# Performance work log

Hardware: AMD Instinct MI355X
Metric: run time of the kernel (lower is better)

The kernel has to match this reference:

```python
import jax, jax.numpy as jnp
import numpy as np

Q, N = 8, 256          # number of sub-networks, state dim per network
QN = Q * N             # 2048 total state dimension
BS = 128               # batch size
TMAX = 128             # time steps
STEP = 0.01            # Euler integration step size


def _offdiag_block_mask(q, n):
    # L_mask: ones everywhere except the q diagonal n x n blocks
    diag_blocks = np.kron(np.eye(q), np.ones((n, n)))
    return jnp.asarray(1.0 - diag_blocks, dtype=jnp.float32)


def setup_inputs() -> dict:
    key = jax.random.key(0)
    ks = jax.random.split(key, 6)
    s = 1.0 / np.sqrt(QN)  # keep 128-step Euler recurrence numerically tame
    X0 = jax.random.normal(ks[0], (BS, QN), dtype=jnp.float32)
    A = jax.random.normal(ks[1], (QN, QN), dtype=jnp.float32) * s
    B = jax.random.normal(ks[2], (QN, QN), dtype=jnp.float32) * s
    W = jax.random.normal(ks[3], (QN, QN), dtype=jnp.float32) * s
    # P is block-diagonal and well-conditioned (I + small block-diag noise)
    blk = np.kron(np.eye(Q), np.ones((N, N))).astype(np.float32)
    P = jnp.eye(QN, dtype=jnp.float32) + 0.1 * jax.random.normal(ks[4], (QN, QN), dtype=jnp.float32) * jnp.asarray(blk)
    bx = jax.random.normal(ks[5], (QN,), dtype=jnp.float32)
    return {"X0": X0, "A": A, "B": B, "W": W, "P": P, "bx": bx, "tmax": TMAX}


def reference(X0, A, B, W, P, bx, tmax):
    # mask GL weight to off-block-diagonal coupling, then L = W - P^{-1} W^T P
    Wm = W * _offdiag_block_mask(Q, N)
    L = Wm - jnp.linalg.solve(P, Wm.T @ P)
    M = A + L                      # (qn, qn)
    Xi0 = X0.T                     # (qn, bs)
    b = bx[:, None]                # (qn, 1) broadcast over batch

    def step_fn(Xi, _):
        Xn = Xi + STEP * (M @ Xi + B @ jax.nn.relu(Xi) + b)
        return Xn, Xn

    _, Xs = jax.lax.scan(step_fn, Xi0, None, length=tmax - 1)  # (tmax-1, qn, bs)
    X = jnp.concatenate([Xi0[None], Xs], axis=0)               # (tmax, qn, bs)
    return jnp.transpose(X, (2, 0, 1))                          # (bs, tmax, qn)
```

## Files before the change

kernel.cpp:

```cpp
#include <hip/hip_runtime.h>

typedef unsigned short u16;
typedef __attribute__((ext_vector_type(8))) short bf16x8;
typedef __attribute__((ext_vector_type(4))) float f32x4;
typedef __attribute__((ext_vector_type(4))) unsigned short u16x4;

#define QN    2048
#define BSZ   128
#define TMAXK 128
#define STEPF 0.01f
#define NEWTON_ITERS 46

#define GLOAD_LDS16(gsrc, ldst) \
  __builtin_amdgcn_global_load_lds((const __attribute__((address_space(1))) void*)(gsrc), \
                                   (__attribute__((address_space(3))) void*)(ldst), 16, 0, 0)

__device__ __forceinline__ u16 f2bf(float f){
  unsigned u = __float_as_uint(f);
  u += 0x7fffu + ((u >> 16) & 1u);
  return (u16)(u >> 16);
}
__device__ __forceinline__ float bf2f(u16 h){
  return __uint_as_float(((unsigned)h) << 16);
}


__global__ __launch_bounds__(256) void alpha_k(const float* __restrict__ P, float* __restrict__ alpha){
  int q = blockIdx.x, i = threadIdx.x;
  const float* Pb = P + (size_t)(q << 8) * QN + (q << 8);
  float rs = 0.f, cs = 0.f;
  for (int c = 0; c < 256; ++c){
    rs += fabsf(Pb[(size_t)i * QN + c]);
    cs += fabsf(Pb[(size_t)c * QN + i]);
  }
  __shared__ float red[256];
  red[i] = rs; __syncthreads();
  for (int o = 128; o > 0; o >>= 1){ if (i < o) red[i] = fmaxf(red[i], red[i+o]); __syncthreads(); }
  float mr = red[0];
  __syncthreads();
  red[i] = cs; __syncthreads();
  for (int o = 128; o > 0; o >>= 1){ if (i < o) red[i] = fmaxf(red[i], red[i+o]); __syncthreads(); }
  if (i == 0) alpha[q] = mr * red[0];
}

__global__ __launch_bounds__(256) void initV_k(const float* __restrict__ P, const float* __restrict__ alpha, float* __restrict__ V){
  int idx = blockIdx.x * 256 + threadIdx.x;
  int q = idx >> 16, rc = idx & 65535;
  int r = rc >> 8, c = rc & 255;
  V[idx] = P[(size_t)((q << 8) + c) * QN + (q << 8) + r] / alpha[q];
}

__global__ __launch_bounds__(256) void newton_TV_k(const float* __restrict__ P,
                                                   const float* __restrict__ Vin,
                                                   float* __restrict__ Vout){
  int q = blockIdx.x >> 4, st = blockIdx.x & 15;
  int cb = st << 4;
  const float* Pb = P + (size_t)(q << 8) * QN + (q << 8);
  const float* Vb = Vin + (q << 16);
  __shared__ float Asm[16][256];
  __shared__ float Bsm[16][16];
  __shared__ float Tb[256][16];
  int tid = threadIdx.x, ty = tid >> 2, tx = tid & 3;
  float acc[4][4];

#pragma unroll
  for (int i = 0; i < 4; i++)
#pragma unroll
    for (int j = 0; j < 4; j++) acc[i][j] = 0.f;
  for (int kb = 0; kb < 256; kb += 16){
    f32x4 av[4];
#pragma unroll
    for (int rd = 0; rd < 4; ++rd){
      int idx = rd * 256 + tid;
      int row = idx >> 2, kq = (idx & 3) << 2;
      av[rd] = *(const f32x4*)(Pb + (size_t)row * QN + kb + kq);
    }
    float bv = Vb[(size_t)(kb + (tid >> 4)) * 256 + cb + (tid & 15)];
    __syncthreads();
#pragma unroll
    for (int rd = 0; rd < 4; ++rd){
      int idx = rd * 256 + tid;
      int row = idx >> 2, kq = (idx & 3) << 2;
#pragma unroll
      for (int u = 0; u < 4; ++u) Asm[kq + u][row] = av[rd][u];
    }
    Bsm[tid >> 4][tid & 15] = bv;
    __syncthreads();
#pragma unroll
    for (int kk = 0; kk < 16; kk++){
      f32x4 a = *(const f32x4*)&Asm[kk][ty << 2];
      f32x4 b = *(const f32x4*)&Bsm[kk][tx << 2];
#pragma unroll
      for (int i = 0; i < 4; i++)
#pragma unroll
        for (int j = 0; j < 4; j++) acc[i][j] += a[i] * b[j];
    }
  }
#pragma unroll
  for (int i = 0; i < 4; i++){
    f32x4 o; o.x = acc[i][0]; o.y = acc[i][1]; o.z = acc[i][2]; o.w = acc[i][3];
    *(f32x4*)&Tb[(ty << 2) + i][tx << 2] = o;
  }

#pragma unroll
  for (int i = 0; i < 4; i++)
#pragma unroll
    for (int j = 0; j < 4; j++) acc[i][j] = 0.f;
  for (int kb = 0; kb < 256; kb += 16){
    f32x4 av[4];
#pragma unroll
    for (int rd = 0; rd < 4; ++rd){
      int idx = rd * 256 + tid;
      int row = idx >> 2, kq = (idx & 3) << 2;
      av[rd] = *(const f32x4*)(Vb + (size_t)row * 256 + kb + kq);
    }
    __syncthreads();
#pragma unroll
    for (int rd = 0; rd < 4; ++rd){
      int idx = rd * 256 + tid;
      int row = idx >> 2, kq = (idx & 3) << 2;
#pragma unroll
      for (int u = 0; u < 4; ++u) Asm[kq + u][row] = av[rd][u];
    }
    __syncthreads();
#pragma unroll
    for (int kk = 0; kk < 16; kk++){
      f32x4 a = *(const f32x4*)&Asm[kk][ty << 2];
      f32x4 b = *(const f32x4*)&Tb[kb + kk][tx << 2];
#pragma unroll
      for (int i = 0; i < 4; i++)
#pragma unroll
        for (int j = 0; j < 4; j++) acc[i][j] += a[i] * b[j];
    }
  }
  float* Ob = Vout + (q << 16);
#pragma unroll
  for (int i = 0; i < 4; i++){
    int row = (ty << 2) + i;
    f32x4 vo = *(const f32x4*)(Vb + (size_t)row * 256 + cb + (tx << 2));
    f32x4 o;
    o.x = 2.f*vo.x - acc[i][0]; o.y = 2.f*vo.y - acc[i][1];
    o.z = 2.f*vo.z - acc[i][2]; o.w = 2.f*vo.w - acc[i][3];
    *(f32x4*)(Ob + (size_t)row * 256 + cb + (tx << 2)) = o;
  }
}

__global__ __launch_bounds__(256) void build_Y_k(const float* __restrict__ W, const float* __restrict__ P, float* __restrict__ Ymat){
  int j  = blockIdx.x >> 7;
  int rt = (blockIdx.x >> 2) & 31;
  int ct = blockIdx.x & 3;
  int rb = rt << 6, cb = ct << 6, jb = j << 8;
  int tid = threadIdx.x, ty = tid >> 4, tx = tid & 15;
  if ((rt >> 2) == j){
#pragma unroll
    for (int i = 0; i < 4; i++){
      f32x4 z = {0.f, 0.f, 0.f, 0.f};
      *(f32x4*)(Ymat + (size_t)(rb + (ty << 2) + i) * QN + jb + cb + (tx << 2)) = z;
    }
    return;
  }
  __shared__ float Asm[16][68];
  __shared__ float Bsm[16][68];
  float acc[4][4];
#pragma unroll
  for (int i = 0; i < 4; i++)
#pragma unroll
    for (int j2 = 0; j2 < 4; j2++) acc[i][j2] = 0.f;
  int sr = tid & 63, sk = tid >> 6;
  for (int kb = 0; kb < 256; kb += 16){
    float a0 = W[(size_t)(jb + kb + sk     ) * QN + rb + sr];
    float a1 = W[(size_t)(jb + kb + sk +  4) * QN + rb + sr];
    float a2 = W[(size_t)(jb + kb + sk +  8) * QN + rb + sr];
    float a3 = W[(size_t)(jb + kb + sk + 12) * QN + rb + sr];
    float b0 = P[(size_t)(jb + kb + sk     ) * QN + jb + cb + sr];
    float b1 = P[(size_t)(jb + kb + sk +  4) * QN + jb + cb + sr];
    float b2 = P[(size_t)(jb + kb + sk +  8) * QN + jb + cb + sr];
    float b3 = P[(size_t)(jb + kb + sk + 12) * QN + jb + cb + sr];
    __syncthreads();
    Asm[sk   ][sr] = a0; Asm[sk+ 4][sr] = a1; Asm[sk+ 8][sr] = a2; Asm[sk+12][sr] = a3;
    Bsm[sk   ][sr] = b0; Bsm[sk+ 4][sr] = b1; Bsm[sk+ 8][sr] = b2; Bsm[sk+12][sr] = b3;
    __syncthreads();
#pragma unroll
    for (int kk = 0; kk < 16; kk++){
      f32x4 a = *(const f32x4*)&Asm[kk][ty << 2];
      f32x4 b = *(const f32x4*)&Bsm[kk][tx << 2];
#pragma unroll
      for (int i = 0; i < 4; i++)
#pragma unroll
        for (int j2 = 0; j2 < 4; j2++) acc[i][j2] += a[i] * b[j2];
    }
  }
#pragma unroll
  for (int i = 0; i < 4; i++){
    f32x4 o; o.x = acc[i][0]; o.y = acc[i][1]; o.z = acc[i][2]; o.w = acc[i][3];
    *(f32x4*)(Ymat + (size_t)(rb + (ty << 2) + i) * QN + jb + cb + (tx << 2)) = o;
  }
}

__global__ __launch_bounds__(256) void build_C_k(const float* __restrict__ Vfin, const float* __restrict__ Ymat,
                                                 const float* __restrict__ Ain, const float* __restrict__ W,
                                                 u16* __restrict__ C1, u16* __restrict__ C2){
  int ib = blockIdx.x >> 7;
  int rest = blockIdx.x & 127;
  int rt = rest >> 5, ct = rest & 31;
  int rb = rt << 6, cb = ct << 6;
  const float* Ab = Vfin + (ib << 16);
  __shared__ float Asm[16][68];
  __shared__ float Bsm[16][68];
  int tid = threadIdx.x, ty = tid >> 4, tx = tid & 15;
  float acc[4][4];
#pragma unroll
  for (int i = 0; i < 4; i++)
#pragma unroll
    for (int j = 0; j < 4; j++) acc[i][j] = 0.f;
  int ar = tid >> 2, ak = (tid & 3) << 2;
  int bc = tid & 63, bk = tid >> 6;
  for (int kb = 0; kb < 256; kb += 16){
    f32x4 av = *(const f32x4*)(Ab + (size_t)(rb + ar) * 256 + kb + ak);
    float b0 = Ymat[(size_t)((ib << 8) + kb + bk     ) * QN + cb + bc];
    float b1 = Ymat[(size_t)((ib << 8) + kb + bk +  4) * QN + cb + bc];
    float b2 = Ymat[(size_t)((ib << 8) + kb + bk +  8) * QN + cb + bc];
    float b3 = Ymat[(size_t)((ib << 8) + kb + bk + 12) * QN + cb + bc];
    __syncthreads();
    Asm[ak+0][ar] = av.x; Asm[ak+1][ar] = av.y; Asm[ak+2][ar] = av.z; Asm[ak+3][ar] = av.w;
    Bsm[bk   ][bc] = b0;  Bsm[bk+ 4][bc] = b1;  Bsm[bk+ 8][bc] = b2;  Bsm[bk+12][bc] = b3;
    __syncthreads();
#pragma unroll
    for (int kk = 0; kk < 16; kk++){
      f32x4 a = *(const f32x4*)&Asm[kk][ty << 2];
      f32x4 b = *(const f32x4*)&Bsm[kk][tx << 2];
#pragma unroll
      for (int i = 0; i < 4; i++)
#pragma unroll
        for (int j = 0; j < 4; j++) acc[i][j] += a[i] * b[j];
    }
  }
#pragma unroll
  for (int i = 0; i < 4; i++){
    int row = (ib << 8) + rb + (ty << 2) + i;
    int sw = (row & 7) << 3;
#pragma unroll
    for (int j = 0; j < 4; j++){
      int col = cb + (tx << 2) + j;
      float wv = ((row >> 8) == (col >> 8)) ? 0.f : W[(size_t)row * QN + col];
      float m = Ain[(size_t)row * QN + col] + wv - acc[i][j];
      u16 hi = f2bf(m);
      u16 lo = f2bf(m - bf2f(hi));
      int colw = col ^ sw;
      C1[((size_t)row << 12) + colw] = hi;
      C2[((size_t)row << 12) + colw] = lo;
    }
  }
}

__global__ __launch_bounds__(256) void split_B_k(const float* __restrict__ Bin, u16* __restrict__ C1, u16* __restrict__ C2){
  int idx = blockIdx.x * 256 + threadIdx.x;
  int r = idx >> 11, c = idx & 2047;
  float v = Bin[idx];
  u16 hi = f2bf(v);
  u16 lo = f2bf(v - bf2f(hi));
  int colw = (2048 + c) ^ ((r & 7) << 3);
  C1[((size_t)r << 12) + colw] = hi;
  C2[((size_t)r << 12) + colw] = lo;
}

__global__ __launch_bounds__(256) void init_state_k(const float* __restrict__ X0, float* __restrict__ Xf,
                                                    u16* __restrict__ Yst, float* __restrict__ out){
  int idx = blockIdx.x * 256 + threadIdx.x;
  int bs = idx >> 11, qn = idx & 2047;
  float x = X0[idx];
  Xf[idx] = x;
  Yst[((size_t)bs << 12) + qn] = f2bf(x);
  Yst[((size_t)bs << 12) + 2048 + qn] = f2bf(fmaxf(x, 0.f));
  out[((size_t)bs * TMAXK) * QN + qn] = x;
}


__global__ __launch_bounds__(256) void step_gemm_k(const u16* __restrict__ C1, const u16* __restrict__ C2,
                                                   const u16* __restrict__ Yst, float* __restrict__ part){
  __shared__ __align__(16) char lds[65536];
  int tid = threadIdx.x;
  int b = blockIdx.x;
  int s = b & 7, rg = b >> 3;
  int k0 = s << 9;
  int w = tid >> 6, l = tid & 63;
#pragma unroll
  for (int it = 0; it < 16; ++it){
    int c = it * 4 + w;
    int p = c >> 5, r = c & 31;
    const u16* src = (p == 0 ? C1 : C2) + ((size_t)((rg << 5) + r) << 12) + k0 + (l << 3);
    GLOAD_LDS16(src, lds + c * 1024);
  }
  __syncthreads();
  int lo16 = l & 15, hi = l >> 4;
  f32x4 acc[2][2];
#pragma unroll
  for (int m = 0; m < 2; m++)
#pragma unroll
    for (int n = 0; n < 2; n++) acc[m][n] = (f32x4){0.f, 0.f, 0.f, 0.f};
  const u16* yb = Yst + ((size_t)((w << 5) + lo16) << 12) + k0 + (hi << 3);
#pragma unroll
  for (int kt = 0; kt < 16; ++kt){
    bf16x8 b0 = *(const bf16x8*)(yb + (kt << 5));
    bf16x8 b1 = *(const bf16x8*)(yb + (16 << 12) + (kt << 5));
    int kb2 = ((kt << 5) + (hi << 3)) << 1;
#pragma unroll
    for (int m = 0; m < 2; m++){
      int row = (m << 4) + lo16;
      int ba = ((row << 10) + kb2) ^ ((row & 7) << 4);
      bf16x8 a1 = *(const bf16x8*)(lds + ba);
      bf16x8 a2 = *(const bf16x8*)(lds + 32768 + ba);
      acc[m][0] = __builtin_amdgcn_mfma_f32_16x16x32_bf16(a1, b0, acc[m][0], 0, 0, 0);
      acc[m][0] = __builtin_amdgcn_mfma_f32_16x16x32_bf16(a2, b0, acc[m][0], 0, 0, 0);
      acc[m][1] = __builtin_amdgcn_mfma_f32_16x16x32_bf16(a1, b1, acc[m][1], 0, 0, 0);
      acc[m][1] = __builtin_amdgcn_mfma_f32_16x16x32_bf16(a2, b1, acc[m][1], 0, 0, 0);
    }
  }
#pragma unroll
  for (int m = 0; m < 2; m++)
#pragma unroll
    for (int n = 0; n < 2; n++){
      int bs = (w << 5) + (n << 4) + lo16;
      int row = (rg << 5) + (m << 4) + (hi << 2);
      __builtin_nontemporal_store(acc[m][n], (f32x4*)(part + ((size_t)((s << 7) + bs) << 11) + row));
    }
}

__global__ __launch_bounds__(256) void step_update_k(const float* __restrict__ part, float* __restrict__ Xf,
                                                     const float* __restrict__ bx, u16* __restrict__ Yst,
                                                     float* __restrict__ out, int t){
  int tid = blockIdx.x * 256 + threadIdx.x;
  int bs = tid >> 9;
  int row = (tid & 511) << 2;
  size_t base = ((size_t)bs << 11) + row;
  f32x4 u = {0.f, 0.f, 0.f, 0.f};
#pragma unroll
  for (int s = 0; s < 8; s++){
    f32x4 p = __builtin_nontemporal_load((const f32x4*)(part + ((size_t)((s << 7) + bs) << 11) + row));
    u += p;
  }
  f32x4 x = *(const f32x4*)(Xf + base);
  f32x4 b = *(const f32x4*)(bx + row);
  f32x4 xn = x + STEPF * (u + b);
  *(f32x4*)(Xf + base) = xn;
  __builtin_nontemporal_store(xn, (f32x4*)(out + ((size_t)((bs << 7) + t) << 11) + row));
  u16x4 hv, rv;
  hv.x = f2bf(xn.x); hv.y = f2bf(xn.y); hv.z = f2bf(xn.z); hv.w = f2bf(xn.w);
  rv.x = f2bf(fmaxf(xn.x, 0.f)); rv.y = f2bf(fmaxf(xn.y, 0.f));
  rv.z = f2bf(fmaxf(xn.z, 0.f)); rv.w = f2bf(fmaxf(xn.w, 0.f));
  *(u16x4*)(Yst + ((size_t)bs << 12) + row) = hv;
  *(u16x4*)(Yst + ((size_t)bs << 12) + 2048 + row) = rv;
}


extern "C" void kernel_launch(void* const* d_in, const int* in_sizes, int n_in,
                              void* d_out, int out_size, void* d_ws, size_t ws_size,
                              hipStream_t stream){
  (void)in_sizes; (void)n_in; (void)out_size; (void)ws_size;
  const float* X0  = (const float*)d_in[0];
  const float* Ain = (const float*)d_in[1];
  const float* Bin = (const float*)d_in[2];
  const float* Win = (const float*)d_in[3];
  const float* Pin = (const float*)d_in[4];
  const float* bx  = (const float*)d_in[5];
  float* out = (float*)d_out;
  char* ws = (char*)d_ws;
  const size_t MB = 1u << 20;

  u16*   C1    = (u16*)(ws);
  u16*   C2    = (u16*)(ws + 16*MB);
  float* Xf    = (float*)(ws + 32*MB);
  u16*   Yst   = (u16*)(ws + 33*MB);
  float* Ymat  = (float*)(ws + 34*MB);
  float* part  = (float*)(ws + 34*MB);
  float* Vb0   = (float*)(ws + 50*MB);
  float* Vb1   = (float*)(ws + 52*MB);
  float* alpha = (float*)(ws + 56*MB);

  alpha_k<<<8, 256, 0, stream>>>(Pin, alpha);
  initV_k<<<2048, 256, 0, stream>>>(Pin, alpha, Vb0);
  float* Vc = Vb0; float* Vo = Vb1;
  for (int it = 0; it < NEWTON_ITERS; ++it){
    newton_TV_k<<<128, 256, 0, stream>>>(Pin, Vc, Vo);
    float* tmp = Vc; Vc = Vo; Vo = tmp;
  }
  build_Y_k<<<1024, 256, 0, stream>>>(Win, Pin, Ymat);
  build_C_k<<<1024, 256, 0, stream>>>(Vc, Ymat, Ain, Win, C1, C2);
  split_B_k<<<16384, 256, 0, stream>>>(Bin, C1, C2);
  init_state_k<<<1024, 256, 0, stream>>>(X0, Xf, Yst, out);

  for (int t = 1; t < TMAXK; ++t){
    step_gemm_k<<<512, 256, 0, stream>>>(C1, C2, Yst, part);
    step_update_k<<<256, 256, 0, stream>>>(part, Xf, bx, Yst, out, t);
  }
}
```

Baseline: 3.709 ms.

## Fuse per-step GEMM and state update into one full-K kernel with ping-pong state

The split-K step GEMM plus separate reduction/update kernel is replaced by one kernel per time step. Each block covers a 32-row tile over the full K=4096 with double-buffered LDS staging, then applies the Euler update directly. The bf16 state buffer is ping-ponged so readers and writers of the same step do not race. This removes the partial-sum round trip through global memory and one launch per step, but drops to 128 blocks of 512 threads, which may underuse the CUs and serializes the K loop inside each block.

```diff
diff --git a/kernel.cpp b/kernel.cpp
--- a/kernel.cpp
+++ b/kernel.cpp
@@ -276,80 +276,67 @@
 }
 
 
-__global__ __launch_bounds__(256) void step_gemm_k(const u16* __restrict__ C1, const u16* __restrict__ C2,
-                                                   const u16* __restrict__ Yst, float* __restrict__ part){
-  __shared__ __align__(16) char lds[65536];
-  int tid = threadIdx.x;
-  int b = blockIdx.x;
-  int s = b & 7, rg = b >> 3;
-  int k0 = s << 9;
+__global__ void __launch_bounds__(512, 1) stepfull_k(
+    const u16* __restrict__ C1, const u16* __restrict__ C2,
+    const u16* __restrict__ YstR, u16* __restrict__ YstW,
+    float* __restrict__ Xf, const float* __restrict__ bx,
+    float* __restrict__ out, int t){
+  extern __shared__ char lds[];
+  int b = blockIdx.x, tid = threadIdx.x;
+  int rt = b & 63, h = b >> 6;
   int w = tid >> 6, l = tid & 63;
-#pragma unroll
-  for (int it = 0; it < 16; ++it){
-    int c = it * 4 + w;
-    int p = c >> 5, r = c & 31;
-    const u16* src = (p == 0 ? C1 : C2) + ((size_t)((rg << 5) + r) << 12) + k0 + (l << 3);
-    GLOAD_LDS16(src, lds + c * 1024);
-  }
+  int lo16 = l & 15, hi = l >> 4;
+  int g = w >> 2, q = w & 3;
+  const int R = rt << 5;
+
+#define STAGE_C(buf, kc) do {                                                  \
+    char* base_ = lds + (buf) * 65536;                                         \
+    _Pragma("unroll")                                                          \
+    for (int it_ = 0; it_ < 8; ++it_){                                         \
+      int c_ = it_ * 8 + w;                                                    \
+      int p_ = c_ >> 5, r_ = c_ & 31;                                          \
+      const u16* src_ = (p_ == 0 ? C1 : C2) +                                  \
+          ((size_t)(R + r_) << 12) + ((kc) << 9) + (l << 3);                   \
+      GLOAD_LDS16(src_, base_ + c_ * 1024);                                    \
+    }                                                                          \
+  } while (0)
+
+  STAGE_C(0, 0);
+  f32x4 acc = {0.f, 0.f, 0.f, 0.f};
+  int rowL = (g << 4) + lo16;
+  int bs = (h << 6) + (q << 4) + lo16;
+  const u16* yb = YstR + ((size_t)bs << 12) + (hi << 3);
   __syncthreads();
-  int lo16 = l & 15, hi = l >> 4;
-  f32x4 acc[2][2];
-#pragma unroll
-  for (int m = 0; m < 2; m++)
-#pragma unroll
-    for (int n = 0; n < 2; n++) acc[m][n] = (f32x4){0.f, 0.f, 0.f, 0.f};
-  const u16* yb = Yst + ((size_t)((w << 5) + lo16) << 12) + k0 + (hi << 3);
-#pragma unroll
-  for (int kt = 0; kt < 16; ++kt){
-    bf16x8 b0 = *(const bf16x8*)(yb + (kt << 5));
-    bf16x8 b1 = *(const bf16x8*)(yb + (16 << 12) + (kt << 5));
-    int kb2 = ((kt << 5) + (hi << 3)) << 1;
-#pragma unroll
-    for (int m = 0; m < 2; m++){
-      int row = (m << 4) + lo16;
-      int ba = ((row << 10) + kb2) ^ ((row & 7) << 4);
-      bf16x8 a1 = *(const bf16x8*)(lds + ba);
-      bf16x8 a2 = *(const bf16x8*)(lds + 32768 + ba);
-      acc[m][0] = __builtin_amdgcn_mfma_f32_16x16x32_bf16(a1, b0, acc[m][0], 0, 0, 0);
-      acc[m][0] = __builtin_amdgcn_mfma_f32_16x16x32_bf16(a2, b0, acc[m][0], 0, 0, 0);
-      acc[m][1] = __builtin_amdgcn_mfma_f32_16x16x32_bf16(a1, b1, acc[m][1], 0, 0, 0);
-      acc[m][1] = __builtin_amdgcn_mfma_f32_16x16x32_bf16(a2, b1, acc[m][1], 0, 0, 0);
-    }
-  }
-#pragma unroll
-  for (int m = 0; m < 2; m++)
-#pragma unroll
-    for (int n = 0; n < 2; n++){
-      int bs = (w << 5) + (n << 4) + lo16;
-      int row = (rg << 5) + (m << 4) + (hi << 2);
-      __builtin_nontemporal_store(acc[m][n], (f32x4*)(part + ((size_t)((s << 7) + bs) << 11) + row));
-    }
-}
-
-__global__ __launch_bounds__(256) void step_update_k(const float* __restrict__ part, float* __restrict__ Xf,
-                                                     const float* __restrict__ bx, u16* __restrict__ Yst,
-                                                     float* __restrict__ out, int t){
-  int tid = blockIdx.x * 256 + threadIdx.x;
-  int bs = tid >> 9;
-  int row = (tid & 511) << 2;
-  size_t base = ((size_t)bs << 11) + row;
-  f32x4 u = {0.f, 0.f, 0.f, 0.f};
-#pragma unroll
-  for (int s = 0; s < 8; s++){
-    f32x4 p = __builtin_nontemporal_load((const f32x4*)(part + ((size_t)((s << 7) + bs) << 11) + row));
-    u += p;
-  }
-  f32x4 x = *(const f32x4*)(Xf + base);
-  f32x4 b = *(const f32x4*)(bx + row);
-  f32x4 xn = x + STEPF * (u + b);
-  *(f32x4*)(Xf + base) = xn;
-  __builtin_nontemporal_store(xn, (f32x4*)(out + ((size_t)((bs << 7) + t) << 11) + row));
+  for (int kc = 0; kc < 8; ++kc){
+    int cur = kc & 1;
+    if (kc < 7) STAGE_C(cur ^ 1, kc + 1);
+    const char* base = lds + cur * 65536;
+#pragma unroll
+    for (int kt = 0; kt < 16; ++kt){
+      bf16x8 b0 = *(const bf16x8*)(yb + (kc << 9) + (kt << 5));
+      int kb2 = ((kt << 5) + (hi << 3)) << 1;
+      int ba = ((rowL << 10) + kb2) ^ ((rowL & 7) << 4);
+      bf16x8 a1 = *(const bf16x8*)(base + ba);
+      bf16x8 a2 = *(const bf16x8*)(base + 32768 + ba);
+      acc = __builtin_amdgcn_mfma_f32_16x16x32_bf16(a1, b0, acc, 0, 0, 0);
+      acc = __builtin_amdgcn_mfma_f32_16x16x32_bf16(a2, b0, acc, 0, 0, 0);
+    }
+    __syncthreads();
+  }
+  int rowg = R + (g << 4) + (hi << 2);
+  size_t xo = ((size_t)bs << 11) + rowg;
+  f32x4 x = *(const f32x4*)(Xf + xo);
+  f32x4 bv = *(const f32x4*)(bx + rowg);
+  f32x4 xn = x + STEPF * (acc + bv);
+  *(f32x4*)(Xf + xo) = xn;
+  __builtin_nontemporal_store(xn, (f32x4*)(out + ((size_t)((bs << 7) + t) << 11) + rowg));
   u16x4 hv, rv;
   hv.x = f2bf(xn.x); hv.y = f2bf(xn.y); hv.z = f2bf(xn.z); hv.w = f2bf(xn.w);
   rv.x = f2bf(fmaxf(xn.x, 0.f)); rv.y = f2bf(fmaxf(xn.y, 0.f));
   rv.z = f2bf(fmaxf(xn.z, 0.f)); rv.w = f2bf(fmaxf(xn.w, 0.f));
-  *(u16x4*)(Yst + ((size_t)bs << 12) + row) = hv;
-  *(u16x4*)(Yst + ((size_t)bs << 12) + 2048 + row) = rv;
+  *(u16x4*)(YstW + ((size_t)bs << 12) + rowg) = hv;
+  *(u16x4*)(YstW + ((size_t)bs << 12) + 2048 + rowg) = rv;
+#undef STAGE_C
 }
 
 
@@ -370,12 +357,12 @@
   u16*   C1    = (u16*)(ws);
   u16*   C2    = (u16*)(ws + 16*MB);
   float* Xf    = (float*)(ws + 32*MB);
-  u16*   Yst   = (u16*)(ws + 33*MB);
+  u16*   Yst0  = (u16*)(ws + 33*MB);
   float* Ymat  = (float*)(ws + 34*MB);
-  float* part  = (float*)(ws + 34*MB);
-  float* Vb0   = (float*)(ws + 50*MB);
-  float* Vb1   = (float*)(ws + 52*MB);
-  float* alpha = (float*)(ws + 56*MB);
+  u16*   Yst1  = (u16*)(ws + 50*MB);
+  float* Vb0   = (float*)(ws + 51*MB);
+  float* Vb1   = (float*)(ws + 53*MB);
+  float* alpha = (float*)(ws + 55*MB);
 
   alpha_k<<<8, 256, 0, stream>>>(Pin, alpha);
   initV_k<<<2048, 256, 0, stream>>>(Pin, alpha, Vb0);
@@ -387,10 +374,12 @@
   build_Y_k<<<1024, 256, 0, stream>>>(Win, Pin, Ymat);
   build_C_k<<<1024, 256, 0, stream>>>(Vc, Ymat, Ain, Win, C1, C2);
   split_B_k<<<16384, 256, 0, stream>>>(Bin, C1, C2);
-  init_state_k<<<1024, 256, 0, stream>>>(X0, Xf, Yst, out);
-
+  init_state_k<<<1024, 256, 0, stream>>>(X0, Xf, Yst0, out);
+
+  hipFuncSetAttribute((const void*)stepfull_k, hipFuncAttributeMaxDynamicSharedMemorySize, 131072);
   for (int t = 1; t < TMAXK; ++t){
-    step_gemm_k<<<512, 256, 0, stream>>>(C1, C2, Yst, part);
-    step_update_k<<<256, 256, 0, stream>>>(part, Xf, bx, Yst, out, t);
-  }
-}
+    const u16* YstR = (t & 1) ? Yst0 : Yst1;
+    u16*       YstW = (t & 1) ? Yst1 : Yst0;
+    stepfull_k<<<128, 512, 131072, stream>>>(C1, C2, YstR, YstW, Xf, bx, out, t);
+  }
+}
```

After: 6.619 ms. 1.78x slower.

## Retile step GEMM to 16-row tiles with 4-way K split and register-staged LDS loads

Applied to the files above, without the earlier changes.

The per-step GEMM now splits K into 4 chunks of 1024 instead of 8 of 512, and each block handles 16 output rows instead of 32. Operand tiles are loaded through registers with the XOR swizzle applied at LDS store time, replacing the direct global-to-LDS loads and the pre-swizzled global layout. The update kernel sums 4 partials instead of 8, which cuts partial-sum traffic. In exchange, each block gets less reuse of the Y operand and a longer serial K loop, and LDS fills now pass through VGPRs.

```diff
diff --git a/kernel.cpp b/kernel.cpp
--- a/kernel.cpp
+++ b/kernel.cpp
@@ -10,10 +10,6 @@
 #define TMAXK 128
 #define STEPF 0.01f
 #define NEWTON_ITERS 46
-
-#define GLOAD_LDS16(gsrc, ldst) \
-  __builtin_amdgcn_global_load_lds((const __attribute__((address_space(1))) void*)(gsrc), \
-                                   (__attribute__((address_space(3))) void*)(ldst), 16, 0, 0)
 
 __device__ __forceinline__ u16 f2bf(float f){
   unsigned u = __float_as_uint(f);
@@ -238,7 +234,6 @@
 #pragma unroll
   for (int i = 0; i < 4; i++){
     int row = (ib << 8) + rb + (ty << 2) + i;
-    int sw = (row & 7) << 3;
 #pragma unroll
     for (int j = 0; j < 4; j++){
       int col = cb + (tx << 2) + j;
@@ -246,9 +241,8 @@
       float m = Ain[(size_t)row * QN + col] + wv - acc[i][j];
       u16 hi = f2bf(m);
       u16 lo = f2bf(m - bf2f(hi));
-      int colw = col ^ sw;
-      C1[((size_t)row << 12) + colw] = hi;
-      C2[((size_t)row << 12) + colw] = lo;
+      C1[((size_t)row << 12) + col] = hi;
+      C2[((size_t)row << 12) + col] = lo;
     }
   }
 }
@@ -259,9 +253,8 @@
   float v = Bin[idx];
   u16 hi = f2bf(v);
   u16 lo = f2bf(v - bf2f(hi));
-  int colw = (2048 + c) ^ ((r & 7) << 3);
-  C1[((size_t)r << 12) + colw] = hi;
-  C2[((size_t)r << 12) + colw] = lo;
+  C1[((size_t)r << 12) + 2048 + c] = hi;
+  C2[((size_t)r << 12) + 2048 + c] = lo;
 }
 
 __global__ __launch_bounds__(256) void init_state_k(const float* __restrict__ X0, float* __restrict__ Xf,
@@ -281,49 +274,45 @@
   __shared__ __align__(16) char lds[65536];
   int tid = threadIdx.x;
   int b = blockIdx.x;
-  int s = b & 7, rg = b >> 3;
-  int k0 = s << 9;
+  int s = b & 3, rg = b >> 2;
+  int k0 = s << 10;
+  int R = rg << 4;
+  for (int it = 0; it < 16; ++it){
+    int e = it * 256 + tid;
+    const u16* src = (e < 2048) ? C1 : C2;
+    int el = e & 2047;
+    int r = el >> 7;
+    int k8 = (el & 127) << 3;
+    bf16x8 v = *(const bf16x8*)(src + ((size_t)(R + r) << 12) + k0 + k8);
+    int addr = ((e >> 11) << 15) + (((r << 11) + (k8 << 1)) ^ ((r & 7) << 4));
+    *(bf16x8*)(lds + addr) = v;
+  }
+  __syncthreads();
   int w = tid >> 6, l = tid & 63;
-#pragma unroll
-  for (int it = 0; it < 16; ++it){
-    int c = it * 4 + w;
-    int p = c >> 5, r = c & 31;
-    const u16* src = (p == 0 ? C1 : C2) + ((size_t)((rg << 5) + r) << 12) + k0 + (l << 3);
-    GLOAD_LDS16(src, lds + c * 1024);
-  }
-  __syncthreads();
   int lo16 = l & 15, hi = l >> 4;
-  f32x4 acc[2][2];
-#pragma unroll
-  for (int m = 0; m < 2; m++)
-#pragma unroll
-    for (int n = 0; n < 2; n++) acc[m][n] = (f32x4){0.f, 0.f, 0.f, 0.f};
-  const u16* yb = Yst + ((size_t)((w << 5) + lo16) << 12) + k0 + (hi << 3);
-#pragma unroll
-  for (int kt = 0; kt < 16; ++kt){
-    bf16x8 b0 = *(const bf16x8*)(yb + (kt << 5));
-    bf16x8 b1 = *(const bf16x8*)(yb + (16 << 12) + (kt << 5));
-    int kb2 = ((kt << 5) + (hi << 3)) << 1;
-#pragma unroll
-    for (int m = 0; m < 2; m++){
-      int row = (m << 4) + lo16;
-      int ba = ((row << 10) + kb2) ^ ((row & 7) << 4);
-      bf16x8 a1 = *(const bf16x8*)(lds + ba);
-      bf16x8 a2 = *(const bf16x8*)(lds + 32768 + ba);
-      acc[m][0] = __builtin_amdgcn_mfma_f32_16x16x32_bf16(a1, b0, acc[m][0], 0, 0, 0);
-      acc[m][0] = __builtin_amdgcn_mfma_f32_16x16x32_bf16(a2, b0, acc[m][0], 0, 0, 0);
-      acc[m][1] = __builtin_amdgcn_mfma_f32_16x16x32_bf16(a1, b1, acc[m][1], 0, 0, 0);
-      acc[m][1] = __builtin_amdgcn_mfma_f32_16x16x32_bf16(a2, b1, acc[m][1], 0, 0, 0);
-    }
-  }
-#pragma unroll
-  for (int m = 0; m < 2; m++)
-#pragma unroll
-    for (int n = 0; n < 2; n++){
-      int bs = (w << 5) + (n << 4) + lo16;
-      int row = (rg << 5) + (m << 4) + (hi << 2);
-      __builtin_nontemporal_store(acc[m][n], (f32x4*)(part + ((size_t)((s << 7) + bs) << 11) + row));
-    }
+  f32x4 acc[2];
+  acc[0] = (f32x4){0.f, 0.f, 0.f, 0.f};
+  acc[1] = (f32x4){0.f, 0.f, 0.f, 0.f};
+  const u16* yb0 = Yst + ((size_t)((w << 5) + lo16) << 12) + k0 + (hi << 3);
+  const u16* yb1 = yb0 + ((size_t)16 << 12);
+#pragma unroll
+  for (int kt = 0; kt < 32; ++kt){
+    bf16x8 b0 = *(const bf16x8*)(yb0 + (kt << 5));
+    bf16x8 b1 = *(const bf16x8*)(yb1 + (kt << 5));
+    int ba = ((lo16 << 11) + (kt << 6) + (hi << 4)) ^ ((lo16 & 7) << 4);
+    bf16x8 a1 = *(const bf16x8*)(lds + ba);
+    bf16x8 a2 = *(const bf16x8*)(lds + 32768 + ba);
+    acc[0] = __builtin_amdgcn_mfma_f32_16x16x32_bf16(a1, b0, acc[0], 0, 0, 0);
+    acc[0] = __builtin_amdgcn_mfma_f32_16x16x32_bf16(a2, b0, acc[0], 0, 0, 0);
+    acc[1] = __builtin_amdgcn_mfma_f32_16x16x32_bf16(a1, b1, acc[1], 0, 0, 0);
+    acc[1] = __builtin_amdgcn_mfma_f32_16x16x32_bf16(a2, b1, acc[1], 0, 0, 0);
+  }
+#pragma unroll
+  for (int n = 0; n < 2; ++n){
+    int bs = (w << 5) + (n << 4) + lo16;
+    int row = R + (hi << 2);
+    __builtin_nontemporal_store(acc[n], (f32x4*)(part + ((size_t)((s << 7) + bs) << 11) + row));
+  }
 }
 
 __global__ __launch_bounds__(256) void step_update_k(const float* __restrict__ part, float* __restrict__ Xf,
@@ -335,7 +324,7 @@
   size_t base = ((size_t)bs << 11) + row;
   f32x4 u = {0.f, 0.f, 0.f, 0.f};
 #pragma unroll
-  for (int s = 0; s < 8; s++){
+  for (int s = 0; s < 4; s++){
     f32x4 p = __builtin_nontemporal_load((const f32x4*)(part + ((size_t)((s << 7) + bs) << 11) + row));
     u += p;
   }
```

Measured after the change: 4.555 ms. 22.8% more time.
